# Optimization experiments

Hardware: AMD Instinct MI355X
Metric: run time of the kernel (lower is better)

Reference implementation:

```python
import jax, jax.numpy as jnp
import numpy as np

B = 2048   # batch
D = 1280   # backbone feature dim (hardcoded in module)
E = 8      # num_classes == number of expert heads
ALPHA = 0.1
EPS = 1e-5


def _bn(x, g, b, m, v):
    # BatchNorm1d in eval mode: running stats
    return (x - m) * jax.lax.rsqrt(v + EPS) * g + b


def _ln(x, g, b):
    mu = jnp.mean(x, axis=-1, keepdims=True)
    var = jnp.mean((x - mu) ** 2, axis=-1, keepdims=True)
    return (x - mu) * jax.lax.rsqrt(var + EPS) * g + b


@jax.custom_vjp
def _grad_reverse(x):
    return x

def _gr_fwd(x):
    return x, None

def _gr_bwd(_, g):
    return (-ALPHA * g,)

_grad_reverse.defvjp(_gr_fwd, _gr_bwd)


def setup_inputs() -> dict:
    key = jax.random.key(0)
    ks = iter(jax.random.split(key, 80))
    def w(*s):
        return jax.random.normal(next(ks), s, dtype=jnp.float32) * 0.02
    def u(*s):
        return jax.random.uniform(next(ks), s, dtype=jnp.float32) + 0.5
    inp = {"source": jax.random.normal(next(ks), (B, D), dtype=jnp.float32)}
    # bottleneck: Linear(1280,512)+BN+ReLU, Linear(512,256)+BN+ReLU
    inp.update(bw1=w(D, 512), bb1=jnp.zeros(512), bg1=jnp.ones(512), bbe1=jnp.zeros(512), bm1=w(512), bv1=u(512))
    inp.update(bw2=w(512, 256), bb2=jnp.zeros(256), bg2=jnp.ones(256), bbe2=jnp.zeros(256), bm2=w(256), bv2=u(256))
    # source_fc: Linear(256, E) + LogSoftmax
    inp.update(cw=w(256, E), cb=jnp.zeros(E))
    # domain classifier: 1280->1024->1024->512->2 with BN
    inp.update(dw1=w(D, 1024), db1=jnp.zeros(1024), dg1=jnp.ones(1024), dbe1=jnp.zeros(1024), dm1=w(1024), dv1=u(1024))
    inp.update(dw2=w(1024, 1024), db2=jnp.zeros(1024), dg2=jnp.ones(1024), dbe2=jnp.zeros(1024), dm2=w(1024), dv2=u(1024))
    inp.update(dw3=w(1024, 512), db3=jnp.zeros(512), dg3=jnp.ones(512), dbe3=jnp.zeros(512), dm3=w(512), dv3=u(512))
    inp.update(dw4=w(512, 2), db4=jnp.zeros(2))
    # E stacked expert MLPs: 1280->1024->1024->512->2 with LayerNorm
    inp.update(ew1=w(E, D, 1024), eb1=jnp.zeros((E, 1024)), eg1=jnp.ones((E, 1024)), ebe1=jnp.zeros((E, 1024)))
    inp.update(ew2=w(E, 1024, 1024), eb2=jnp.zeros((E, 1024)), eg2=jnp.ones((E, 1024)), ebe2=jnp.zeros((E, 1024)))
    inp.update(ew3=w(E, 1024, 512), eb3=jnp.zeros((E, 512)), eg3=jnp.ones((E, 512)), ebe3=jnp.zeros((E, 512)))
    inp.update(ew4=w(E, 512, 2), eb4=jnp.zeros((E, 2)))
    return inp


def reference(source, bw1, bb1, bg1, bbe1, bm1, bv1, bw2, bb2, bg2, bbe2, bm2, bv2, cw, cb,
              dw1, db1, dg1, dbe1, dm1, dv1, dw2, db2, dg2, dbe2, dm2, dv2,
              dw3, db3, dg3, dbe3, dm3, dv3, dw4, db4,
              ew1, eb1, eg1, ebe1, ew2, eb2, eg2, ebe2, ew3, eb3, eg3, ebe3, ew4, eb4):
    share = source  # sharedNet modeled as identity on extracted features
    # bottleneck + classifier head
    h = jax.nn.relu(_bn(share @ bw1 + bb1, bg1, bbe1, bm1, bv1))
    h = jax.nn.relu(_bn(h @ bw2 + bb2, bg2, bbe2, bm2, bv2))
    src = jax.nn.log_softmax(h @ cw + cb, axis=-1)            # [B, E]
    label = jnp.argmax(src, axis=-1)                          # routing labels (detached by argmax)
    # gradient-reversed features
    rev = _grad_reverse(share)
    # global domain classifier (dropout = identity in eval)
    d = jax.nn.relu(_bn(rev @ dw1 + db1, dg1, dbe1, dm1, dv1))
    d = jax.nn.relu(_bn(d @ dw2 + db2, dg2, dbe2, dm2, dv2))
    d = jax.nn.relu(_bn(d @ dw3 + db3, dg3, dbe3, dm3, dv3))
    dclf = jax.nn.log_softmax(d @ dw4 + db4, axis=-1)         # [B, 2]
    # per-class domain experts: dense all-expert compute + per-sample gather
    x = jax.nn.relu(_ln(jnp.einsum('bd,edh->beh', rev, ew1) + eb1[None], eg1[None], ebe1[None]))
    x = jax.nn.relu(_ln(jnp.einsum('beh,ehk->bek', x, ew2) + eb2[None], eg2[None], ebe2[None]))
    x = jax.nn.relu(_ln(jnp.einsum('beh,ehk->bek', x, ew3) + eb3[None], eg3[None], ebe3[None]))
    eo = jax.nn.log_softmax(jnp.einsum('beh,ehk->bek', x, ew4) + eb4[None], axis=-1)  # [B, E, 2]
    sout = jnp.take_along_axis(eo, label[:, None, None], axis=1)[:, 0, :]             # [B, 2]
    return (src, dclf, sout, share)
```

## Files before the change

kernel.cpp:

```cpp
#include <hip/hip_runtime.h>

typedef unsigned short u16;
typedef short s8v __attribute__((ext_vector_type(8)));
typedef float f4v __attribute__((ext_vector_type(4)));

#define AS1 __attribute__((address_space(1)))
#define AS3 __attribute__((address_space(3)))

__device__ __forceinline__ float bf2f(u16 u) {
    union { unsigned int i; float f; } x; x.i = ((unsigned int)u) << 16; return x.f;
}
__device__ __forceinline__ u16 f2bf(float f) {
    union { float f; unsigned int i; } x; x.f = f;
    unsigned int r = x.i + 0x7fffu + ((x.i >> 16) & 1u);
    return (u16)(r >> 16);
}

__device__ __forceinline__ void glds16(const u16* g, u16* l) {
    __builtin_amdgcn_global_load_lds((AS1 void*)(g), (AS3 void*)(l), 16, 0, 0);
}

__device__ __forceinline__ int swz(int row, int kq) {
    return row * 64 + ((((kq >> 3) ^ row) & 7) << 3);
}

__global__ __launch_bounds__(256) void convsrc_k(const float* __restrict__ in,
        u16* __restrict__ outb, float* __restrict__ outf, int n8)
{
    const int i = blockIdx.x * 256 + threadIdx.x;
    if (i >= n8) return;
    const float4 f0 = ((const float4*)in)[i * 2];
    const float4 f1 = ((const float4*)in)[i * 2 + 1];
    s8v v;
    v[0]=(short)f2bf(f0.x); v[1]=(short)f2bf(f0.y);
    v[2]=(short)f2bf(f0.z); v[3]=(short)f2bf(f0.w);
    v[4]=(short)f2bf(f1.x); v[5]=(short)f2bf(f1.y);
    v[6]=(short)f2bf(f1.z); v[7]=(short)f2bf(f1.w);
    ((s8v*)outb)[i] = v;
    ((float4*)outf)[i * 2]     = f0;
    ((float4*)outf)[i * 2 + 1] = f1;
}

template<int HASDOM>
__global__ __launch_bounds__(512) void gemm_btf_k(
    const u16* __restrict__ A0, size_t aStrideZ,
    const float* __restrict__ Wa, const float* __restrict__ Wb, int zSplit,
    const float* __restrict__ ebias,
    const float* __restrict__ dbias, const float* __restrict__ dgam,
    const float* __restrict__ dbet,  const float* __restrict__ dmean,
    const float* __restrict__ dvar,  int zdom,
    u16* __restrict__ out0, int M, int N, int K)
{
    const int z = blockIdx.z;
    const u16* A = A0 + (size_t)z * aStrideZ;
    const float* W = (z < zSplit) ? Wa + (size_t)z * K * N
                                  : Wb + (size_t)(z - zSplit) * K * N;
    u16* out = out0 + (size_t)z * M * N;

    const int n0 = blockIdx.x * 128, m0 = blockIdx.y * 128;
    const int t = threadIdx.x;
    const int w = t >> 6, lane = t & 63;
    const int lq = lane >> 4, lr = lane & 15;
    const int wm = (w >> 1) * 32;
    const int wn = (w & 1) * 64;

    __shared__ __align__(16) u16 As[2 * 8192];
    __shared__ __align__(16) u16 Bs[2 * 8192];

    f4v acc[2][4] = {};

    const int srow = t >> 3;
    const u16* ga = A + (size_t)(m0 + srow) * K + (((t & 7) ^ (srow & 7)) << 3);
    const int wq = w * 512;
    const int rowK = 64 * K;

#define AGLDS(buf, kk) do { \
    glds16(ga + (kk),        As + (buf) * 8192 + wq); \
    glds16(ga + (kk) + rowK, As + (buf) * 8192 + 4096 + wq); } while (0)

    const int nl = t & 127;
    const int kb = (t >> 7) << 4;
    const float* wp0 = W + (size_t)kb * N + n0 + nl;
    const int bofs0 = nl * 64 + (((( kb >> 3)      ^ nl) & 7) << 3);
    const int bofs1 = nl * 64 + (((((kb >> 3) + 1) ^ nl) & 7) << 3);

    const int NT = K >> 6;
    float bv[16];

    {
        #pragma unroll
        for (int i = 0; i < 16; ++i) bv[i] = wp0[(size_t)i * N];
        AGLDS(0, 0);
        s8v pk0, pk1;
        #pragma unroll
        for (int i = 0; i < 8; ++i) { pk0[i] = (short)f2bf(bv[i]); pk1[i] = (short)f2bf(bv[8 + i]); }
        *(s8v*)&Bs[bofs0] = pk0;
        *(s8v*)&Bs[bofs1] = pk1;
    }

    for (int tk = 0; tk < NT; ++tk) {
        const int cur = tk & 1;
        if (tk + 1 < NT) {
            const float* wp = wp0 + (size_t)(tk + 1) * 64 * N;
            #pragma unroll
            for (int i = 0; i < 16; ++i) bv[i] = wp[(size_t)i * N];
            AGLDS(cur ^ 1, (tk + 1) << 6);
            s8v pk0, pk1;
            #pragma unroll
            for (int i = 0; i < 8; ++i) { pk0[i] = (short)f2bf(bv[i]); pk1[i] = (short)f2bf(bv[8 + i]); }
            u16* bb = Bs + (cur ^ 1) * 8192;
            *(s8v*)&bb[bofs0] = pk0;
            *(s8v*)&bb[bofs1] = pk1;
        } else {
            asm volatile("s_waitcnt vmcnt(0)" ::: "memory");
        }
        asm volatile("s_waitcnt lgkmcnt(0)" ::: "memory");
        __builtin_amdgcn_s_barrier();
        __builtin_amdgcn_sched_barrier(0);

        const u16* Ah = As + cur * 8192;
        const u16* Bh = Bs + cur * 8192;
        __builtin_amdgcn_s_setprio(1);
        #pragma unroll
        for (int ks = 0; ks < 64; ks += 32) {
            const int kq = ks + (lq << 3);
            s8v a[2], b[4];
            #pragma unroll
            for (int i = 0; i < 2; ++i) a[i] = *(const s8v*)&Ah[swz(wm + i*16 + lr, kq)];
            #pragma unroll
            for (int j = 0; j < 4; ++j) b[j] = *(const s8v*)&Bh[swz(wn + j*16 + lr, kq)];
            #pragma unroll
            for (int i = 0; i < 2; ++i)
                #pragma unroll
                for (int j = 0; j < 4; ++j)
                    acc[i][j] = __builtin_amdgcn_mfma_f32_16x16x32_bf16(a[i], b[j], acc[i][j], 0, 0, 0);
        }
        __builtin_amdgcn_s_setprio(0);
        __builtin_amdgcn_sched_barrier(0);
        __builtin_amdgcn_s_barrier();
    }
#undef AGLDS

    float scale[4], shift[4];
    const bool dom = HASDOM && (z == zdom);
    #pragma unroll
    for (int j = 0; j < 4; ++j) {
        const int c = n0 + wn + j * 16 + lr;
        if (dom) {
            const float s = dgam[c] / sqrtf(dvar[c] + 1e-5f);
            scale[j] = s;
            shift[j] = (dbias[c] - dmean[c]) * s + dbet[c];
        } else {
            scale[j] = 1.f;
            shift[j] = ebias[(size_t)z * N + c];
        }
    }
    const int r0 = lq << 2;
    #pragma unroll
    for (int i = 0; i < 2; ++i) {
        #pragma unroll
        for (int r = 0; r < 4; ++r) {
            const int grow = m0 + wm + i * 16 + r0 + r;
            u16* orow = out + (size_t)grow * N + n0 + wn + lr;
            #pragma unroll
            for (int j = 0; j < 4; ++j) {
                float y = fmaf(acc[i][j][r], scale[j], shift[j]);
                if (dom) y = fmaxf(y, 0.f);
                orow[j * 16] = f2bf(y);
            }
        }
    }
}

__global__ __launch_bounds__(256) void gemm_f32sk_k(
    const float* __restrict__ A, const float* __restrict__ W,
    float* __restrict__ out, int M, int N, int K, int Ks)
{
    const int n0 = blockIdx.x * 128, m0 = blockIdx.y * 64;
    const int kb = blockIdx.z * Ks;
    out += (size_t)blockIdx.z * M * N;
    const int t = threadIdx.x;
    const int tx = t & 15, ty = t >> 4;
    __shared__ float As[64 * 33];
    __shared__ float Bs[32 * 132];
    float acc[4][8] = {};
    const int ar = t >> 2, akc = (t & 3) * 8;
    const int bk = t >> 3, bnc = (t & 7) * 16;
    for (int kk = kb; kk < kb + Ks; kk += 32) {
        const float* ap = A + (size_t)(m0 + ar) * K + kk + akc;
        const float4 fa0 = *(const float4*)(ap);
        const float4 fa1 = *(const float4*)(ap + 4);
        float* asp = &As[ar * 33 + akc];
        asp[0] = fa0.x; asp[1] = fa0.y; asp[2] = fa0.z; asp[3] = fa0.w;
        asp[4] = fa1.x; asp[5] = fa1.y; asp[6] = fa1.z; asp[7] = fa1.w;
        const float* wp = W + (size_t)(kk + bk) * N + n0 + bnc;
        #pragma unroll
        for (int q = 0; q < 4; ++q)
            *(float4*)&Bs[bk * 132 + bnc + q * 4] = *(const float4*)(wp + q * 4);
        __syncthreads();
        #pragma unroll 8
        for (int kq = 0; kq < 32; ++kq) {
            float a[4];
            #pragma unroll
            for (int i = 0; i < 4; ++i) a[i] = As[(ty + 16 * i) * 33 + kq];
            const float4 b0 = *(const float4*)&Bs[kq * 132 + tx * 4];
            const float4 b1 = *(const float4*)&Bs[kq * 132 + tx * 4 + 64];
            #pragma unroll
            for (int i = 0; i < 4; ++i) {
                acc[i][0] = fmaf(a[i], b0.x, acc[i][0]);
                acc[i][1] = fmaf(a[i], b0.y, acc[i][1]);
                acc[i][2] = fmaf(a[i], b0.z, acc[i][2]);
                acc[i][3] = fmaf(a[i], b0.w, acc[i][3]);
                acc[i][4] = fmaf(a[i], b1.x, acc[i][4]);
                acc[i][5] = fmaf(a[i], b1.y, acc[i][5]);
                acc[i][6] = fmaf(a[i], b1.z, acc[i][6]);
                acc[i][7] = fmaf(a[i], b1.w, acc[i][7]);
            }
        }
        __syncthreads();
    }
    #pragma unroll
    for (int i = 0; i < 4; ++i) {
        float* orow = out + (size_t)(m0 + ty + 16 * i) * N + n0 + tx * 4;
        float4 o0; o0.x = acc[i][0]; o0.y = acc[i][1]; o0.z = acc[i][2]; o0.w = acc[i][3];
        float4 o1; o1.x = acc[i][4]; o1.y = acc[i][5]; o1.z = acc[i][6]; o1.w = acc[i][7];
        *(float4*)orow = o0;
        *(float4*)(orow + 64) = o1;
    }
}

__global__ __launch_bounds__(256) void h2gemm_k(
    const float* __restrict__ hp,
    const float* __restrict__ bg1, const float* __restrict__ bbe1,
    const float* __restrict__ bb1, const float* __restrict__ bm1,
    const float* __restrict__ bv1,
    const float* __restrict__ bw2,
    float* __restrict__ out, int B)
{
    const int n0 = blockIdx.x * 64, m0 = blockIdx.y * 64;
    const int kb = blockIdx.z * 128;
    out += (size_t)blockIdx.z * B * 256;
    const size_t sl = (size_t)B * 512;
    const int tid = threadIdx.x;
    const int tx = tid & 15, ty = tid >> 4;
    __shared__ float As[64][65];
    __shared__ float Bs[64][64];
    __shared__ __align__(16) float scl[128], shl[128];
    if (tid < 128) {
        const int k = kb + tid;
        const float sc = bg1[k] / sqrtf(bv1[k] + 1e-5f);
        scl[tid] = sc;
        shl[tid] = (bb1[k] - bm1[k]) * sc + bbe1[k];
    }
    __syncthreads();
    float acc[4][4] = {};
    const int sr = tid >> 2;
    const int sc = (tid & 3) << 4;
    for (int kk = kb; kk < kb + 128; kk += 64) {
        const int kl = kk - kb;
        const float* ap = hp + (size_t)(m0 + sr) * 512 + kk + sc;
        #pragma unroll
        for (int q = 0; q < 4; ++q) {
            float vx = 0.f, vy = 0.f, vz = 0.f, vw = 0.f;
            #pragma unroll
            for (int s = 0; s < 8; ++s) {
                const float4 f = *(const float4*)(ap + (size_t)s * sl + q * 4);
                vx += f.x; vy += f.y; vz += f.z; vw += f.w;
            }
            const float4 g = *(const float4*)&scl[kl + sc + q * 4];
            const float4 h = *(const float4*)&shl[kl + sc + q * 4];
            As[sr][sc + q*4 + 0] = fmaxf(fmaf(vx, g.x, h.x), 0.f);
            As[sr][sc + q*4 + 1] = fmaxf(fmaf(vy, g.y, h.y), 0.f);
            As[sr][sc + q*4 + 2] = fmaxf(fmaf(vz, g.z, h.z), 0.f);
            As[sr][sc + q*4 + 3] = fmaxf(fmaf(vw, g.w, h.w), 0.f);
        }
        const float* wp = bw2 + (size_t)(kk + sr) * 256 + n0 + sc;
        #pragma unroll
        for (int q = 0; q < 4; ++q)
            *(float4*)&Bs[sr][sc + q*4] = *(const float4*)(wp + q * 4);
        __syncthreads();
        #pragma unroll 4
        for (int kq = 0; kq < 64; ++kq) {
            float a[4], bv[4];
            #pragma unroll
            for (int i = 0; i < 4; ++i) a[i] = As[ty*4 + i][kq];
            #pragma unroll
            for (int j = 0; j < 4; ++j) bv[j] = Bs[kq][tx*4 + j];
            #pragma unroll
            for (int i = 0; i < 4; ++i)
                #pragma unroll
                for (int j = 0; j < 4; ++j)
                    acc[i][j] = fmaf(a[i], bv[j], acc[i][j]);
        }
        __syncthreads();
    }
    #pragma unroll
    for (int j = 0; j < 4; ++j) {
        const int c = n0 + tx*4 + j;
        #pragma unroll
        for (int i = 0; i < 4; ++i)
            out[(size_t)(m0 + ty*4 + i) * 256 + c] = acc[i][j];
    }
}

__global__ __launch_bounds__(256) void cls_k(
    const float* __restrict__ h2p,
    const float* __restrict__ bg2, const float* __restrict__ bbe2,
    const float* __restrict__ bb2, const float* __restrict__ bm2,
    const float* __restrict__ bv2,
    const float* __restrict__ cw,  const float* __restrict__ cb,
    float* __restrict__ out_src, int* __restrict__ label, int B)
{
    const int b = blockIdx.x * 4 + (threadIdx.x >> 6);
    const int lane = threadIdx.x & 63;
    const size_t sl = (size_t)B * 256;
    const float* hb = h2p + (size_t)b * 256 + lane * 4;
    const float4 v0 = *(const float4*)(hb);
    const float4 v1 = *(const float4*)(hb + sl);
    const float4 v2 = *(const float4*)(hb + 2 * sl);
    const float4 v3 = *(const float4*)(hb + 3 * sl);
    const float4 gv = ((const float4*)bg2)[lane];
    const float4 vv = ((const float4*)bv2)[lane];
    const float4 bbv = ((const float4*)bb2)[lane];
    const float4 bmv = ((const float4*)bm2)[lane];
    const float4 bev = ((const float4*)bbe2)[lane];
    float h[4];
    {
        const float s0 = gv.x / sqrtf(vv.x + 1e-5f);
        const float s1 = gv.y / sqrtf(vv.y + 1e-5f);
        const float s2 = gv.z / sqrtf(vv.z + 1e-5f);
        const float s3 = gv.w / sqrtf(vv.w + 1e-5f);
        h[0] = fmaxf(fmaf(v0.x + v1.x + v2.x + v3.x, s0, (bbv.x - bmv.x) * s0 + bev.x), 0.f);
        h[1] = fmaxf(fmaf(v0.y + v1.y + v2.y + v3.y, s1, (bbv.y - bmv.y) * s1 + bev.y), 0.f);
        h[2] = fmaxf(fmaf(v0.z + v1.z + v2.z + v3.z, s2, (bbv.z - bmv.z) * s2 + bev.z), 0.f);
        h[3] = fmaxf(fmaf(v0.w + v1.w + v2.w + v3.w, s3, (bbv.w - bmv.w) * s3 + bev.w), 0.f);
    }
    float p[8] = {};
    #pragma unroll
    for (int j = 0; j < 4; ++j) {
        const float4 c0 = ((const float4*)cw)[(lane * 4 + j) * 2];
        const float4 c1 = ((const float4*)cw)[(lane * 4 + j) * 2 + 1];
        p[0] = fmaf(h[j], c0.x, p[0]); p[1] = fmaf(h[j], c0.y, p[1]);
        p[2] = fmaf(h[j], c0.z, p[2]); p[3] = fmaf(h[j], c0.w, p[3]);
        p[4] = fmaf(h[j], c1.x, p[4]); p[5] = fmaf(h[j], c1.y, p[5]);
        p[6] = fmaf(h[j], c1.z, p[6]); p[7] = fmaf(h[j], c1.w, p[7]);
    }
    #pragma unroll
    for (int off = 32; off; off >>= 1)
        #pragma unroll
        for (int c = 0; c < 8; ++c) p[c] += __shfl_xor(p[c], off, 64);
    if (lane == 0) {
        float lg[8];
        #pragma unroll
        for (int c = 0; c < 8; ++c) lg[c] = p[c] + cb[c];
        float mx = lg[0]; int am = 0;
        #pragma unroll
        for (int c = 1; c < 8; ++c) if (lg[c] > mx) { mx = lg[c]; am = c; }
        float ssum = 0.f;
        #pragma unroll
        for (int c = 0; c < 8; ++c) ssum += expf(lg[c] - mx);
        const float lse = mx + logf(ssum);
        #pragma unroll
        for (int c = 0; c < 8; ++c) out_src[b * 8 + c] = lg[c] - lse;
        label[b] = am;
    }
}

template<int N>
__global__ __launch_bounds__(256) void ln_relu_k(u16* __restrict__ Y,
        const float* __restrict__ g, const float* __restrict__ bb)
{
    const int z = blockIdx.y;
    u16* y = Y + ((size_t)z * gridDim.x + blockIdx.x) * N;
    const float* gz = g  + (size_t)z * N;
    const float* bz = bb + (size_t)z * N;
    const int t = threadIdx.x;
    constexpr int C = N >> 8;
    float vals[C];
    ushort4 u = ((const ushort4*)y)[t];
    vals[0] = bf2f(u.x); vals[1] = bf2f(u.y);
    vals[2] = bf2f(u.z); vals[3] = bf2f(u.w);
    float s = 0.f, sq = 0.f;
    #pragma unroll
    for (int i = 0; i < C; ++i) { s += vals[i]; sq += vals[i] * vals[i]; }
    #pragma unroll
    for (int off = 32; off; off >>= 1) {
        s  += __shfl_xor(s,  off, 64);
        sq += __shfl_xor(sq, off, 64);
    }
    __shared__ float rs[4], rq[4];
    if ((t & 63) == 0) { rs[t >> 6] = s; rq[t >> 6] = sq; }
    __syncthreads();
    s  = rs[0] + rs[1] + rs[2] + rs[3];
    sq = rq[0] + rq[1] + rq[2] + rq[3];
    const float inv = 1.f / (float)N;
    const float mu  = s * inv;
    const float var = sq * inv - mu * mu;
    const float rstd = rsqrtf(var + 1e-5f);
    float4 gv = ((const float4*)gz)[t];
    float4 bv = ((const float4*)bz)[t];
    ushort4 o;
    o.x = f2bf(fmaxf((vals[0] - mu) * rstd * gv.x + bv.x, 0.f));
    o.y = f2bf(fmaxf((vals[1] - mu) * rstd * gv.y + bv.y, 0.f));
    o.z = f2bf(fmaxf((vals[2] - mu) * rstd * gv.z + bv.z, 0.f));
    o.w = f2bf(fmaxf((vals[3] - mu) * rstd * gv.w + bv.w, 0.f));
    ((ushort4*)y)[t] = o;
}

__global__ __launch_bounds__(64) void headsel_k(
    const u16* __restrict__ X,
    const int* __restrict__ label,
    const float* __restrict__ eg3, const float* __restrict__ ebe3,
    const float* __restrict__ ew4, const float* __restrict__ eb4,
    int zBase, float* __restrict__ out_sout, int B)
{
    const int b = blockIdx.x;
    const int e = label[b];
    if (e < zBase || e >= zBase + 4) return;
    const int lane = threadIdx.x;
    const u16* x = X + ((size_t)(e - zBase) * B + b) * 512 + lane * 8;
    uint4 raw = *(const uint4*)x;
    const u16* pu = (const u16*)&raw;
    float v[8];
    #pragma unroll
    for (int i = 0; i < 8; ++i) v[i] = bf2f(pu[i]);
    float s = 0.f, sq = 0.f;
    #pragma unroll
    for (int i = 0; i < 8; ++i) { s += v[i]; sq += v[i] * v[i]; }
    #pragma unroll
    for (int off = 32; off; off >>= 1) {
        s  += __shfl_xor(s,  off, 64);
        sq += __shfl_xor(sq, off, 64);
    }
    const float mu = s * (1.f / 512.f);
    const float var = sq * (1.f / 512.f) - mu * mu;
    const float rstd = rsqrtf(var + 1e-5f);
    const float* g  = eg3  + (size_t)e * 512 + lane * 8;
    const float* be = ebe3 + (size_t)e * 512 + lane * 8;
    const float4 g0 = *(const float4*)g,  g1 = *(const float4*)(g + 4);
    const float4 b0 = *(const float4*)be, b1 = *(const float4*)(be + 4);
    float h[8];
    h[0] = fmaxf((v[0]-mu)*rstd*g0.x + b0.x, 0.f);
    h[1] = fmaxf((v[1]-mu)*rstd*g0.y + b0.y, 0.f);
    h[2] = fmaxf((v[2]-mu)*rstd*g0.z + b0.z, 0.f);
    h[3] = fmaxf((v[3]-mu)*rstd*g0.w + b0.w, 0.f);
    h[4] = fmaxf((v[4]-mu)*rstd*g1.x + b1.x, 0.f);
    h[5] = fmaxf((v[5]-mu)*rstd*g1.y + b1.y, 0.f);
    h[6] = fmaxf((v[6]-mu)*rstd*g1.z + b1.z, 0.f);
    h[7] = fmaxf((v[7]-mu)*rstd*g1.w + b1.w, 0.f);
    const float* W = ew4 + (size_t)e * 1024 + lane * 16;
    float p0 = 0.f, p1 = 0.f;
    #pragma unroll
    for (int q = 0; q < 4; ++q) {
        const float4 wv = *(const float4*)(W + q * 4);
        p0 = fmaf(h[q*2],   wv.x, p0); p1 = fmaf(h[q*2],   wv.y, p1);
        p0 = fmaf(h[q*2+1], wv.z, p0); p1 = fmaf(h[q*2+1], wv.w, p1);
    }
    #pragma unroll
    for (int off = 32; off; off >>= 1) {
        p0 += __shfl_xor(p0, off, 64);
        p1 += __shfl_xor(p1, off, 64);
    }
    if (lane == 0) {
        const float l0 = p0 + eb4[e * 2];
        const float l1 = p1 + eb4[e * 2 + 1];
        const float mx = fmaxf(l0, l1);
        const float lse = mx + logf(expf(l0 - mx) + expf(l1 - mx));
        out_sout[b * 2]     = l0 - lse;
        out_sout[b * 2 + 1] = l1 - lse;
    }
}

__global__ __launch_bounds__(64) void head2_k(const u16* __restrict__ X,
        const float* __restrict__ W, const float* __restrict__ bias,
        float* __restrict__ out)
{
    const int b = blockIdx.x;
    const int lane = threadIdx.x;
    const u16* x = X + (size_t)b * 512 + lane * 8;
    uint4 raw = *(const uint4*)x;
    const u16* pu = (const u16*)&raw;
    const float* Wz = W + lane * 16;
    float p0 = 0.f, p1 = 0.f;
    #pragma unroll
    for (int q = 0; q < 4; ++q) {
        const float4 wv = *(const float4*)(Wz + q * 4);
        p0 = fmaf(bf2f(pu[q*2]),   wv.x, p0); p1 = fmaf(bf2f(pu[q*2]),   wv.y, p1);
        p0 = fmaf(bf2f(pu[q*2+1]), wv.z, p0); p1 = fmaf(bf2f(pu[q*2+1]), wv.w, p1);
    }
    #pragma unroll
    for (int off = 32; off; off >>= 1) {
        p0 += __shfl_xor(p0, off, 64);
        p1 += __shfl_xor(p1, off, 64);
    }
    if (lane == 0) {
        const float l0 = p0 + bias[0];
        const float l1 = p1 + bias[1];
        const float mx = fmaxf(l0, l1);
        const float lse = mx + logf(expf(l0 - mx) + expf(l1 - mx));
        out[b * 2]     = l0 - lse;
        out[b * 2 + 1] = l1 - lse;
    }
}


extern "C" void kernel_launch(void* const* d_in, const int* in_sizes, int n_in,
                              void* d_out, int out_size, void* d_ws, size_t ws_size,
                              hipStream_t stream)
{
    const int B = 2048, D = 1280, E = 8;

    const float* src = (const float*)d_in[0];
    const float *bw1 = (const float*)d_in[1],  *bb1 = (const float*)d_in[2],
                *bg1 = (const float*)d_in[3],  *bbe1 = (const float*)d_in[4],
                *bm1 = (const float*)d_in[5],  *bv1 = (const float*)d_in[6];
    const float *bw2 = (const float*)d_in[7],  *bb2 = (const float*)d_in[8],
                *bg2 = (const float*)d_in[9],  *bbe2 = (const float*)d_in[10],
                *bm2 = (const float*)d_in[11], *bv2 = (const float*)d_in[12];
    const float *cw  = (const float*)d_in[13], *cb  = (const float*)d_in[14];
    const float *dw1 = (const float*)d_in[15], *db1 = (const float*)d_in[16],
                *dg1 = (const float*)d_in[17], *dbe1 = (const float*)d_in[18],
                *dm1 = (const float*)d_in[19], *dv1 = (const float*)d_in[20];
    const float *dw2 = (const float*)d_in[21], *db2 = (const float*)d_in[22],
                *dg2 = (const float*)d_in[23], *dbe2 = (const float*)d_in[24],
                *dm2 = (const float*)d_in[25], *dv2 = (const float*)d_in[26];
    const float *dw3 = (const float*)d_in[27], *db3 = (const float*)d_in[28],
                *dg3 = (const float*)d_in[29], *dbe3 = (const float*)d_in[30],
                *dm3 = (const float*)d_in[31], *dv3 = (const float*)d_in[32];
    const float *dw4 = (const float*)d_in[33], *db4 = (const float*)d_in[34];
    const float *ew1 = (const float*)d_in[35], *eb1 = (const float*)d_in[36],
                *eg1 = (const float*)d_in[37], *ebe1 = (const float*)d_in[38];
    const float *ew2 = (const float*)d_in[39], *eb2 = (const float*)d_in[40],
                *eg2 = (const float*)d_in[41], *ebe2 = (const float*)d_in[42];
    const float *ew3 = (const float*)d_in[43], *eb3 = (const float*)d_in[44],
                *eg3 = (const float*)d_in[45], *ebe3 = (const float*)d_in[46];
    const float *ew4 = (const float*)d_in[47], *eb4 = (const float*)d_in[48];

    float* out_src   = (float*)d_out;
    float* out_dclf  = out_src + B * E;
    float* out_sout  = out_dclf + B * 2;
    float* out_share = out_sout + B * 2;

    char* ws = (char*)d_ws;
    u16*   srcb  = (u16*)(ws + 13107200);
    u16*   acta  = (u16*)(ws + 18350080);
    u16*   actb  = (u16*)(ws + 39321600);
    int*   label = (int*)(ws + 60293120);
    float* hp    = (float*)(ws + 18350080);
    float* h2p   = (float*)(ws);

    const size_t s1024 = (size_t)B * 1024, s512 = (size_t)B * 512;

    convsrc_k<<<dim3(B * D / 8 / 256), 256, 0, stream>>>(src, srcb, out_share, B * D / 8);

    gemm_f32sk_k<<<dim3(512 / 128, B / 64, 8), 256, 0, stream>>>(
        src, bw1, hp, B, 512, D, 160);
    h2gemm_k<<<dim3(256 / 64, B / 64, 4), 256, 0, stream>>>(
        hp, bg1, bbe1, bb1, bm1, bv1, bw2, h2p, B);
    cls_k<<<dim3(B / 4), 256, 0, stream>>>(
        h2p, bg2, bbe2, bb2, bm2, bv2, cw, cb, out_src, label, B);

    gemm_btf_k<1><<<dim3(8, 16, 5), 512, 0, stream>>>(
        srcb, 0, ew1, dw1, 4, eb1, db1, dg1, dbe1, dm1, dv1, 4, acta, B, 1024, 1280);
    ln_relu_k<1024><<<dim3(B, 4), 256, 0, stream>>>(acta, eg1, ebe1);

    gemm_btf_k<1><<<dim3(8, 16, 5), 512, 0, stream>>>(
        acta, s1024, ew2, dw2, 4, eb2, db2, dg2, dbe2, dm2, dv2, 4, actb, B, 1024, 1024);
    ln_relu_k<1024><<<dim3(B, 4), 256, 0, stream>>>(actb, eg2, ebe2);

    gemm_btf_k<1><<<dim3(4, 16, 5), 512, 0, stream>>>(
        actb, s1024, ew3, dw3, 4, eb3, db3, dg3, dbe3, dm3, dv3, 4, acta, B, 512, 1024);

    headsel_k<<<dim3(B), 64, 0, stream>>>(
        acta, label, eg3, ebe3, ew4, eb4, 0, out_sout, B);
    head2_k<<<dim3(B), 64, 0, stream>>>(
        acta + (size_t)4 * s512, dw4, db4, out_dclf);

    gemm_btf_k<0><<<dim3(8, 16, 4), 512, 0, stream>>>(
        srcb, 0, ew1 + (size_t)4*1280*1024, ew1 + (size_t)4*1280*1024, 4,
        eb1 + (size_t)4*1024, nullptr, nullptr, nullptr, nullptr, nullptr, -1,
        acta, B, 1024, 1280);
    ln_relu_k<1024><<<dim3(B, 4), 256, 0, stream>>>(acta, eg1 + (size_t)4*1024, ebe1 + (size_t)4*1024);

    gemm_btf_k<0><<<dim3(8, 16, 4), 512, 0, stream>>>(
        acta, s1024, ew2 + (size_t)4*1024*1024, ew2 + (size_t)4*1024*1024, 4,
        eb2 + (size_t)4*1024, nullptr, nullptr, nullptr, nullptr, nullptr, -1,
        actb, B, 1024, 1024);
    ln_relu_k<1024><<<dim3(B, 4), 256, 0, stream>>>(actb, eg2 + (size_t)4*1024, ebe2 + (size_t)4*1024);

    gemm_btf_k<0><<<dim3(4, 16, 4), 512, 0, stream>>>(
        actb, s1024, ew3 + (size_t)4*1024*512, ew3 + (size_t)4*1024*512, 4,
        eb3 + (size_t)4*512, nullptr, nullptr, nullptr, nullptr, nullptr, -1,
        acta, B, 512, 1024);

    headsel_k<<<dim3(B), 64, 0, stream>>>(
        acta, label, eg3, ebe3, ew4, eb4, 4, out_sout, B);
}
```

Measured before the change: 632.4 us.

## Prefetch fp32 weights two tiles ahead and halve split-K in bottleneck GEMM

```diff
diff --git a/kernel.cpp b/kernel.cpp
--- a/kernel.cpp
+++ b/kernel.cpp
@@ -80,40 +80,40 @@
 
     const int nl = t & 127;
     const int kb = (t >> 7) << 4;
-    const float* wp0 = W + (size_t)kb * N + n0 + nl;
+    const float* Wp = W + (size_t)kb * N + n0 + nl;
     const int bofs0 = nl * 64 + (((( kb >> 3)      ^ nl) & 7) << 3);
     const int bofs1 = nl * 64 + (((((kb >> 3) + 1) ^ nl) & 7) << 3);
 
+#define LOADB(dst, tkk) do { \
+    const float* wp_ = Wp + (size_t)(tkk) * 64 * N; \
+    _Pragma("unroll") \
+    for (int i_ = 0; i_ < 16; ++i_) dst[i_] = wp_[(size_t)i_ * N]; } while (0)
+
+#define CONVW(srcv, bb) do { \
+    s8v p0_, p1_; \
+    _Pragma("unroll") \
+    for (int i_ = 0; i_ < 8; ++i_) { \
+        p0_[i_] = (short)f2bf(srcv[i_]); p1_[i_] = (short)f2bf(srcv[8 + i_]); } \
+    *(s8v*)&(bb)[bofs0] = p0_; \
+    *(s8v*)&(bb)[bofs1] = p1_; } while (0)
+
     const int NT = K >> 6;
-    float bv[16];
-
-    {
-        #pragma unroll
-        for (int i = 0; i < 16; ++i) bv[i] = wp0[(size_t)i * N];
-        AGLDS(0, 0);
-        s8v pk0, pk1;
-        #pragma unroll
-        for (int i = 0; i < 8; ++i) { pk0[i] = (short)f2bf(bv[i]); pk1[i] = (short)f2bf(bv[8 + i]); }
-        *(s8v*)&Bs[bofs0] = pk0;
-        *(s8v*)&Bs[bofs1] = pk1;
-    }
+    float bvA[16], bvB[16];
+
+    LOADB(bvA, 0);
+    AGLDS(0, 0);
+    CONVW(bvA, Bs);
+    if (NT > 1) LOADB(bvB, 1);
 
     for (int tk = 0; tk < NT; ++tk) {
         const int cur = tk & 1;
-        if (tk + 1 < NT) {
-            const float* wp = wp0 + (size_t)(tk + 1) * 64 * N;
-            #pragma unroll
-            for (int i = 0; i < 16; ++i) bv[i] = wp[(size_t)i * N];
-            AGLDS(cur ^ 1, (tk + 1) << 6);
-            s8v pk0, pk1;
-            #pragma unroll
-            for (int i = 0; i < 8; ++i) { pk0[i] = (short)f2bf(bv[i]); pk1[i] = (short)f2bf(bv[8 + i]); }
-            u16* bb = Bs + (cur ^ 1) * 8192;
-            *(s8v*)&bb[bofs0] = pk0;
-            *(s8v*)&bb[bofs1] = pk1;
-        } else {
-            asm volatile("s_waitcnt vmcnt(0)" ::: "memory");
-        }
+        if (tk + 2 < NT) { if ((tk & 1) == 0) LOADB(bvA, tk + 2); else LOADB(bvB, tk + 2); }
+        if (tk + 1 < NT) AGLDS(cur ^ 1, (tk + 1) << 6);
+
+        if (tk == 0)           asm volatile("s_waitcnt vmcnt(34)" ::: "memory");
+        else if (tk < NT - 2)  asm volatile("s_waitcnt vmcnt(18)" ::: "memory");
+        else if (tk == NT - 2) asm volatile("s_waitcnt vmcnt(2)"  ::: "memory");
+        else                   asm volatile("s_waitcnt vmcnt(0)"  ::: "memory");
         asm volatile("s_waitcnt lgkmcnt(0)" ::: "memory");
         __builtin_amdgcn_s_barrier();
         __builtin_amdgcn_sched_barrier(0);
@@ -137,9 +137,16 @@
         }
         __builtin_amdgcn_s_setprio(0);
         __builtin_amdgcn_sched_barrier(0);
+
+        if (tk + 1 < NT) {
+            u16* bb = Bs + (cur ^ 1) * 8192;
+            if ((tk & 1) == 0) { CONVW(bvB, bb); } else { CONVW(bvA, bb); }
+        }
         __builtin_amdgcn_s_barrier();
     }
 #undef AGLDS
+#undef LOADB
+#undef CONVW
 
     float scale[4], shift[4];
     const bool dom = HASDOM && (z == zdom);
@@ -261,18 +268,16 @@
         const float* ap = hp + (size_t)(m0 + sr) * 512 + kk + sc;
         #pragma unroll
         for (int q = 0; q < 4; ++q) {
-            float vx = 0.f, vy = 0.f, vz = 0.f, vw = 0.f;
-            #pragma unroll
-            for (int s = 0; s < 8; ++s) {
-                const float4 f = *(const float4*)(ap + (size_t)s * sl + q * 4);
-                vx += f.x; vy += f.y; vz += f.z; vw += f.w;
-            }
+            const float4 f0 = *(const float4*)(ap + q * 4);
+            const float4 f1 = *(const float4*)(ap + sl + q * 4);
+            const float4 f2 = *(const float4*)(ap + 2 * sl + q * 4);
+            const float4 f3 = *(const float4*)(ap + 3 * sl + q * 4);
             const float4 g = *(const float4*)&scl[kl + sc + q * 4];
             const float4 h = *(const float4*)&shl[kl + sc + q * 4];
-            As[sr][sc + q*4 + 0] = fmaxf(fmaf(vx, g.x, h.x), 0.f);
-            As[sr][sc + q*4 + 1] = fmaxf(fmaf(vy, g.y, h.y), 0.f);
-            As[sr][sc + q*4 + 2] = fmaxf(fmaf(vz, g.z, h.z), 0.f);
-            As[sr][sc + q*4 + 3] = fmaxf(fmaf(vw, g.w, h.w), 0.f);
+            As[sr][sc + q*4 + 0] = fmaxf(fmaf(f0.x + f1.x + f2.x + f3.x, g.x, h.x), 0.f);
+            As[sr][sc + q*4 + 1] = fmaxf(fmaf(f0.y + f1.y + f2.y + f3.y, g.y, h.y), 0.f);
+            As[sr][sc + q*4 + 2] = fmaxf(fmaf(f0.z + f1.z + f2.z + f3.z, g.z, h.z), 0.f);
+            As[sr][sc + q*4 + 3] = fmaxf(fmaf(f0.w + f1.w + f2.w + f3.w, g.w, h.w), 0.f);
         }
         const float* wp = bw2 + (size_t)(kk + sr) * 256 + n0 + sc;
         #pragma unroll
@@ -553,8 +558,8 @@
 
     convsrc_k<<<dim3(B * D / 8 / 256), 256, 0, stream>>>(src, srcb, out_share, B * D / 8);
 
-    gemm_f32sk_k<<<dim3(512 / 128, B / 64, 8), 256, 0, stream>>>(
-        src, bw1, hp, B, 512, D, 160);
+    gemm_f32sk_k<<<dim3(512 / 128, B / 64, 4), 256, 0, stream>>>(
+        src, bw1, hp, B, 512, D, 320);
     h2gemm_k<<<dim3(256 / 64, B / 64, 4), 256, 0, stream>>>(
         hp, bg1, bbe1, bb1, bm1, bv1, bw2, h2p, B);
     cls_k<<<dim3(B / 4), 256, 0, stream>>>(
```

Result: slower. 753.6 us (+19.2%).
